# Optimization experiments

Hardware: AMD Instinct MI355X
Metric: run time of the kernel (lower is better)

## Reference

```python
import jax, jax.numpy as jnp
import numpy as np

D_MODEL = 512
N_LAYERS = 4
VOCAB = 256
SEQ = 2048
BATCH = 8
EPS = 1e-5


def _ln(x, g, b):
    mu = jnp.mean(x, axis=-1, keepdims=True)
    var = jnp.mean(jnp.square(x - mu), axis=-1, keepdims=True)
    return (x - mu) * jax.lax.rsqrt(var + EPS) * g + b


def setup_inputs() -> dict:
    key = jax.random.key(0)
    ks = jax.random.split(key, 16)
    d, dff = D_MODEL, 4 * D_MODEL
    s = 0.02
    inp = {
        "tokens": jax.random.randint(ks[0], (BATCH, SEQ), 0, VOCAB, dtype=jnp.int64),
        "emb": jax.random.normal(ks[1], (VOCAB, d), jnp.float32) * s,
        "W_upd": jax.random.normal(ks[2], (d, d), jnp.float32) * s,
        "b_upd": jnp.zeros((d,), jnp.float32),
        "W_f": jax.random.normal(ks[3], (d, d), jnp.float32) * s,
        "b_f": jnp.zeros((d,), jnp.float32),
        "decay_param": jnp.zeros((1,), jnp.float32),
        "norm_g": jnp.ones((d,), jnp.float32),
        "norm_b": jnp.zeros((d,), jnp.float32),
        "cms_ln_g": jnp.ones((N_LAYERS, d), jnp.float32),
        "cms_ln_b": jnp.zeros((N_LAYERS, d), jnp.float32),
        "cms_W1": jax.random.normal(ks[4], (N_LAYERS, d, dff), jnp.float32) * s,
        "cms_b1": jnp.zeros((N_LAYERS, dff), jnp.float32),
        "cms_W2": jax.random.normal(ks[5], (N_LAYERS, dff, d), jnp.float32) * s,
        "cms_b2": jnp.zeros((N_LAYERS, d), jnp.float32),
        "head_W": jax.random.normal(ks[6], (d, VOCAB), jnp.float32) * s,
        "head_b": jnp.zeros((VOCAB,), jnp.float32),
    }
    return inp


def _fast_memory(x, mask, W_upd, b_upd, W_f, b_f, decay_param):
    # x: (B,S,d), mask: (B,S) float
    decay = jax.nn.sigmoid(decay_param[0])
    u = jnp.einsum("bsd,de->bse", x, W_upd) + b_upd  # precompute updates
    u_t = jnp.swapaxes(u, 0, 1)                        # (S,B,d)
    m_t = jnp.swapaxes(mask, 0, 1)[..., None]          # (S,B,1)

    def step(mem, inp):
        u_i, msk = inp
        new = decay * mem + u_i
        mem = msk * new + (1.0 - msk) * mem
        return mem, mem

    mem0 = jnp.zeros((x.shape[0], x.shape[2]), x.dtype)
    _, mems = jax.lax.scan(step, mem0, (u_t, m_t))     # (S,B,d)
    mems = jnp.swapaxes(mems, 0, 1)                    # (B,S,d)
    return jnp.einsum("bsd,de->bse", mems, W_f) + b_f


def reference(tokens, emb, W_upd, b_upd, W_f, b_f, decay_param, norm_g, norm_b,
              cms_ln_g, cms_ln_b, cms_W1, cms_b1, cms_W2, cms_b2, head_W, head_b):
    mask = (tokens != 0).astype(emb.dtype)
    x = emb[tokens]                                    # (B,S,d)
    x = x + _fast_memory(x, mask, W_upd, b_upd, W_f, b_f, decay_param)
    x = _ln(x, norm_g, norm_b)
    for i in range(N_LAYERS):
        h = _ln(x, cms_ln_g[i], cms_ln_b[i])
        h = jax.nn.gelu(jnp.einsum("bsd,df->bsf", h, cms_W1[i]) + cms_b1[i], approximate=False)
        h = jnp.einsum("bsf,fd->bsd", h, cms_W2[i]) + cms_b2[i]
        x = x + h
    return jnp.einsum("bsd,dv->bsv", x, head_W) + head_b
```

## Files before the change

### kernel.cpp

```cpp
#include <hip/hip_runtime.h>
#include <hip/hip_bf16.h>
#include <math.h>

#define D_MODEL 512
#define N_LAYERS 4
#define SEQ 2048
#define BATCH 8
#define M_TOT (BATCH * SEQ)
#define DFF 2048
#define HEAD_V 256
#define SC 32
#define NC (SEQ / SC)

typedef __hip_bfloat16 bf16;
typedef __bf16 bf16x8 __attribute__((ext_vector_type(8)));
typedef float f32x4 __attribute__((ext_vector_type(4)));

__device__ __forceinline__ unsigned short bfbits(float x) {
    bf16 h = __float2bfloat16(x);
    return *(unsigned short*)&h;
}
__device__ __forceinline__ unsigned int pk(float a, float b) {
    return (unsigned int)bfbits(a) | ((unsigned int)bfbits(b) << 16);
}

__global__ void convT_kernel(const float* __restrict__ W, bf16* __restrict__ WT,
                             int R, int C, size_t wstride, size_t tstride) {
    W += (size_t)blockIdx.z * wstride;
    WT += (size_t)blockIdx.z * tstride;
    __shared__ float t[32][33];
    int r0 = blockIdx.x * 32, c0 = blockIdx.y * 32;
    int tx = threadIdx.x, ty = threadIdx.y;
    #pragma unroll
    for (int i = 0; i < 32; i += 8)
        t[ty + i][tx] = W[(size_t)(r0 + ty + i) * C + c0 + tx];
    __syncthreads();
    #pragma unroll
    for (int i = 0; i < 32; i += 8)
        WT[(size_t)(c0 + ty + i) * R + r0 + tx] = __float2bfloat16(t[tx][ty + i]);
}

__global__ void embed_kernel(const int* __restrict__ tokens,
                             const float* __restrict__ emb,
                             float* __restrict__ xf, bf16* __restrict__ xb) {
    int row = blockIdx.x, t = threadIdx.x;
    int tok = tokens[row];
    float4 v = ((const float4*)(emb + (size_t)tok * D_MODEL))[t];
    ((float4*)(xf + (size_t)row * D_MODEL))[t] = v;
    uint2 st; st.x = pk(v.x, v.y); st.y = pk(v.z, v.w);
    ((uint2*)(xb + (size_t)row * D_MODEL))[t] = st;
}

__global__ void scanA_kernel(bf16* __restrict__ u, const int* __restrict__ tokens,
                             const float* __restrict__ decayp,
                             float* __restrict__ L, float* __restrict__ P) {
    int idx = blockIdx.x;
    int dblk = idx & 1;
    int c = (idx >> 1) & (NC - 1);
    int b = idx >> 7;
    int d = dblk * 256 + threadIdx.x;
    float decay = 1.0f / (1.0f + __expf(-decayp[0]));
    const int* tok = tokens + (size_t)b * SEQ + c * SC;
    bf16* up = u + ((size_t)b * SEQ + (size_t)c * SC) * D_MODEL + d;
    float mem = 0.0f;
    #pragma unroll 4
    for (int s = 0; s < SC; ++s) {
        float ui = __bfloat162float(up[(size_t)s * D_MODEL]);
        bool m = (tok[s] != 0);
        mem = (m ? decay : 1.0f) * mem + (m ? ui : 0.0f);
        up[(size_t)s * D_MODEL] = __float2bfloat16(mem);
    }
    L[((size_t)b * NC + c) * D_MODEL + d] = mem;
    if (threadIdx.x == 0 && dblk == 0) {
        int cnt = 0;
        for (int s = 0; s < SC; ++s) cnt += (tok[s] != 0);
        P[b * NC + c] = __powf(decay, (float)cnt);
    }
}

__global__ void scanB_kernel(const float* __restrict__ L, const float* __restrict__ P,
                             float* __restrict__ Mc) {
    int b = blockIdx.x >> 1;
    int d = (blockIdx.x & 1) * 256 + threadIdx.x;
    float carry = 0.0f;
    for (int c = 0; c < NC; ++c) {
        size_t off = ((size_t)b * NC + c) * D_MODEL + d;
        Mc[off] = carry;
        carry = P[b * NC + c] * carry + L[off];
    }
}

__global__ void scanC_kernel(bf16* __restrict__ u, const int* __restrict__ tokens,
                             const float* __restrict__ decayp,
                             const float* __restrict__ Mc) {
    int idx = blockIdx.x;
    int dblk = idx & 1;
    int c = (idx >> 1) & (NC - 1);
    int b = idx >> 7;
    if (c == 0) return;
    int d = dblk * 256 + threadIdx.x;
    float decay = 1.0f / (1.0f + __expf(-decayp[0]));
    const int* tok = tokens + (size_t)b * SEQ + c * SC;
    bf16* up = u + ((size_t)b * SEQ + (size_t)c * SC) * D_MODEL + d;
    float carry = Mc[((size_t)b * NC + c) * D_MODEL + d];
    float coeff = 1.0f;
    #pragma unroll 4
    for (int s = 0; s < SC; ++s) {
        bool m = (tok[s] != 0);
        coeff *= (m ? decay : 1.0f);
        float local = __bfloat162float(up[(size_t)s * D_MODEL]);
        up[(size_t)s * D_MODEL] = __float2bfloat16(local + carry * coeff);
    }
}

template <int WF, int WB>
__global__ void ln_kernel(const float* __restrict__ in, float* __restrict__ outf,
                          bf16* __restrict__ outb, const float* __restrict__ g,
                          const float* __restrict__ b) {
    int w = threadIdx.x >> 6, lane = threadIdx.x & 63;
    int row = blockIdx.x * 4 + w;
    const float4* ip = (const float4*)(in + (size_t)row * D_MODEL);
    float4 v0 = ip[lane * 2], v1 = ip[lane * 2 + 1];
    float s1 = v0.x + v0.y + v0.z + v0.w + v1.x + v1.y + v1.z + v1.w;
    float s2 = v0.x * v0.x + v0.y * v0.y + v0.z * v0.z + v0.w * v0.w +
               v1.x * v1.x + v1.y * v1.y + v1.z * v1.z + v1.w * v1.w;
    #pragma unroll
    for (int off = 32; off; off >>= 1) {
        s1 += __shfl_xor(s1, off);
        s2 += __shfl_xor(s2, off);
    }
    float mu = s1 * (1.0f / D_MODEL);
    float var = s2 * (1.0f / D_MODEL) - mu * mu;
    float rstd = rsqrtf(var + 1e-5f);
    const float4* g4 = (const float4*)g;
    const float4* b4 = (const float4*)b;
    float4 g0 = g4[lane * 2], g1 = g4[lane * 2 + 1];
    float4 b0 = b4[lane * 2], b1 = b4[lane * 2 + 1];
    float4 o0, o1;
    o0.x = (v0.x - mu) * rstd * g0.x + b0.x;
    o0.y = (v0.y - mu) * rstd * g0.y + b0.y;
    o0.z = (v0.z - mu) * rstd * g0.z + b0.z;
    o0.w = (v0.w - mu) * rstd * g0.w + b0.w;
    o1.x = (v1.x - mu) * rstd * g1.x + b1.x;
    o1.y = (v1.y - mu) * rstd * g1.y + b1.y;
    o1.z = (v1.z - mu) * rstd * g1.z + b1.z;
    o1.w = (v1.w - mu) * rstd * g1.w + b1.w;
    if (WF) {
        float4* op = (float4*)(outf + (size_t)row * D_MODEL);
        op[lane * 2] = o0; op[lane * 2 + 1] = o1;
    }
    if (WB) {
        uint4 st;
        st.x = pk(o0.x, o0.y); st.y = pk(o0.z, o0.w);
        st.z = pk(o1.x, o1.y); st.w = pk(o1.z, o1.w);
        ((uint4*)(outb + (size_t)row * D_MODEL))[lane] = st;
    }
}

template <int BN, int GELU, int RES, int OBF>
__launch_bounds__(256)
__global__ void gemm_bf16(const bf16* __restrict__ A, const bf16* __restrict__ BT,
                          const float* __restrict__ bias, const float* __restrict__ R,
                          float* __restrict__ Cf, bf16* __restrict__ Cb,
                          int N, int K) {
    constexpr int NJ = BN / 32;
    __shared__ bf16 As[128 * 32];
    __shared__ bf16 Bs[BN * 32];
    const int tid = threadIdx.x;
    const int lane = tid & 63;
    const int w = tid >> 6, wr = w >> 1, wc = w & 1;
    const int lm = lane & 15, lk = lane >> 4;
    const int m0 = blockIdx.x * 128, n0 = blockIdx.y * BN;

    f32x4 acc[4][NJ] = {};

    for (int k0 = 0; k0 < K; k0 += 32) {
        #pragma unroll
        for (int it = 0; it < 2; ++it) {
            int c = tid + it * 256;
            __builtin_amdgcn_global_load_lds(
                A + (size_t)(m0 + (c >> 2)) * K + k0 + (c & 3) * 8,
                (char*)As + (c & ~63) * 16, 16, 0, 0);
        }
        #pragma unroll
        for (int it = 0; it < BN / 64; ++it) {
            int c = tid + it * 256;
            __builtin_amdgcn_global_load_lds(
                BT + (size_t)(n0 + (c >> 2)) * K + k0 + (c & 3) * 8,
                (char*)Bs + (c & ~63) * 16, 16, 0, 0);
        }
        __syncthreads();
        bf16x8 fa[4], fb[NJ];
        #pragma unroll
        for (int i = 0; i < 4; ++i)
            fa[i] = *(const bf16x8*)(As + (wr * 64 + i * 16 + lm) * 32 + lk * 8);
        #pragma unroll
        for (int j = 0; j < NJ; ++j)
            fb[j] = *(const bf16x8*)(Bs + (wc * (BN / 2) + j * 16 + lm) * 32 + lk * 8);
        #pragma unroll
        for (int i = 0; i < 4; ++i)
            #pragma unroll
            for (int j = 0; j < NJ; ++j)
                acc[i][j] = __builtin_amdgcn_mfma_f32_16x16x32_bf16(fa[i], fb[j], acc[i][j], 0, 0, 0);
        __syncthreads();
    }

    #pragma unroll
    for (int j = 0; j < NJ; ++j) {
        int col = n0 + wc * (BN / 2) + j * 16 + lm;
        float bv = bias[col];
        #pragma unroll
        for (int i = 0; i < 4; ++i) {
            int rbase = m0 + wr * 64 + i * 16 + lk * 4;
            #pragma unroll
            for (int r = 0; r < 4; ++r) {
                float v = acc[i][j][r] + bv;
                if (GELU) v = 0.5f * v * (1.0f + erff(v * 0.70710678118654752f));
                size_t off = (size_t)(rbase + r) * N + col;
                if (RES) v += R[off];
                if (OBF == 1) {
                    Cb[off] = __float2bfloat16(v);
                } else if (OBF == 2) {
                    Cf[off] = v;
                    Cb[off] = __float2bfloat16(v);
                } else {
                    Cf[off] = v;
                }
            }
        }
    }
}

extern "C" void kernel_launch(void* const* d_in, const int* in_sizes, int n_in,
                              void* d_out, int out_size, void* d_ws, size_t ws_size,
                              hipStream_t stream) {
    const int*   tokens = (const int*)d_in[0];
    const float* emb    = (const float*)d_in[1];
    const float* W_upd  = (const float*)d_in[2];
    const float* b_upd  = (const float*)d_in[3];
    const float* W_f    = (const float*)d_in[4];
    const float* b_f    = (const float*)d_in[5];
    const float* decayp = (const float*)d_in[6];
    const float* norm_g = (const float*)d_in[7];
    const float* norm_b = (const float*)d_in[8];
    const float* cms_g  = (const float*)d_in[9];
    const float* cms_b  = (const float*)d_in[10];
    const float* cW1    = (const float*)d_in[11];
    const float* cb1    = (const float*)d_in[12];
    const float* cW2    = (const float*)d_in[13];
    const float* cb2    = (const float*)d_in[14];
    const float* head_W = (const float*)d_in[15];
    const float* head_b = (const float*)d_in[16];
    float* out = (float*)d_out;

    const int M = M_TOT, D = D_MODEL, F = DFF, V = HEAD_V;

    float* xf = (float*)d_ws;
    bf16*  lnb = (bf16*)((char*)d_ws + (size_t)M * D * 4);
    bf16*  wb  = (bf16*)((char*)lnb + (size_t)M * D * 2);
    const size_t WB_ELEMS = 9043968;
    char* dyn = (char*)wb + WB_ELEMS * 2;
    size_t used = (size_t)(dyn - (char*)d_ws);
    size_t avail = ws_size > used ? ws_size - used : 0;
    int MC = 4096;
    if (avail >= (size_t)16384 * F * 2) MC = 16384;
    else if (avail >= (size_t)8192 * F * 2) MC = 8192;
    bf16* ub = (bf16*)dyn;
    bf16* hb = (bf16*)dyn;

    float* scanL = out;
    float* scanM = out + (size_t)BATCH * NC * D;
    float* scanP = scanM + (size_t)BATCH * NC * D;

    bf16* WupdT = wb;
    bf16* WfT   = wb + 262144;
    bf16* W1T   = wb + 524288;
    bf16* W2T   = wb + 4718592;
    bf16* HWT   = wb + 8912896;

    dim3 tb(32, 8);
    convT_kernel<<<dim3(16, 16, 2), tb, 0, stream>>>(W_upd, WupdT, D, D,
                                                     (size_t)(W_f - W_upd), 262144);
    convT_kernel<<<dim3(16, 64, N_LAYERS), tb, 0, stream>>>(cW1, W1T, D, F,
                                                            (size_t)D * F, 1048576);
    convT_kernel<<<dim3(64, 16, N_LAYERS), tb, 0, stream>>>(cW2, W2T, F, D,
                                                            (size_t)F * D, 1048576);
    convT_kernel<<<dim3(16, 8, 1), tb, 0, stream>>>(head_W, HWT, D, V, 0, 0);

    embed_kernel<<<M, 128, 0, stream>>>(tokens, emb, xf, lnb);

    gemm_bf16<128, 0, 0, 1><<<dim3(M / 128, D / 128), 256, 0, stream>>>(
        lnb, WupdT, b_upd, nullptr, nullptr, ub, D, D);
    scanA_kernel<<<BATCH * NC * 2, 256, 0, stream>>>(ub, tokens, decayp, scanL, scanP);
    scanB_kernel<<<BATCH * 2, 256, 0, stream>>>(scanL, scanP, scanM);
    scanC_kernel<<<BATCH * NC * 2, 256, 0, stream>>>(ub, tokens, decayp, scanM);
    gemm_bf16<128, 0, 1, 0><<<dim3(M / 128, D / 128), 256, 0, stream>>>(
        ub, WfT, b_f, xf, xf, nullptr, D, D);
    ln_kernel<1, 0><<<M / 4, 256, 0, stream>>>(xf, xf, nullptr, norm_g, norm_b);

    for (int l = 0; l < N_LAYERS; ++l) {
        ln_kernel<0, 1><<<M / 4, 256, 0, stream>>>(xf, nullptr, lnb,
                                                   cms_g + (size_t)l * D,
                                                   cms_b + (size_t)l * D);
        bool last = (l == N_LAYERS - 1);
        for (int mc = 0; mc < M; mc += MC) {
            gemm_bf16<128, 1, 0, 1><<<dim3(MC / 128, F / 128), 256, 0, stream>>>(
                lnb + (size_t)mc * D, W1T + (size_t)l * 1048576,
                cb1 + (size_t)l * F, nullptr, nullptr, hb, F, D);
            if (MC >= 8192) {
                if (last)
                    gemm_bf16<128, 0, 1, 2><<<dim3(MC / 128, D / 128), 256, 0, stream>>>(
                        hb, W2T + (size_t)l * 1048576, cb2 + (size_t)l * D,
                        xf + (size_t)mc * D, xf + (size_t)mc * D,
                        lnb + (size_t)mc * D, D, F);
                else
                    gemm_bf16<128, 0, 1, 0><<<dim3(MC / 128, D / 128), 256, 0, stream>>>(
                        hb, W2T + (size_t)l * 1048576, cb2 + (size_t)l * D,
                        xf + (size_t)mc * D, xf + (size_t)mc * D, nullptr, D, F);
            } else {
                if (last)
                    gemm_bf16<64, 0, 1, 2><<<dim3(MC / 128, D / 64), 256, 0, stream>>>(
                        hb, W2T + (size_t)l * 1048576, cb2 + (size_t)l * D,
                        xf + (size_t)mc * D, xf + (size_t)mc * D,
                        lnb + (size_t)mc * D, D, F);
                else
                    gemm_bf16<64, 0, 1, 0><<<dim3(MC / 128, D / 64), 256, 0, stream>>>(
                        hb, W2T + (size_t)l * 1048576, cb2 + (size_t)l * D,
                        xf + (size_t)mc * D, xf + (size_t)mc * D, nullptr, D, F);
            }
        }
    }

    gemm_bf16<128, 0, 0, 0><<<dim3(M / 128, V / 128), 256, 0, stream>>>(
        lnb, HWT, head_b, nullptr, out, nullptr, V, D);
}
```

Before: 660.5 us.

## Double-buffer GEMM LDS tiles and stage epilogue through LDS for vector stores

The GEMM main loop now keeps two LDS buffers and prefetches the next K tile with global_load_lds while MFMAs run on the current one. This replaces the two __syncthreads per iteration with a single wait plus barrier. The epilogue writes each warp's accumulators to LDS, then reads them back row-contiguous so bias, residual and outputs use float4 and uint4 accesses instead of scalar strided ones. The change doubles shared memory per block, which may reduce occupancy. Template kernels are also wrapped into named non-template kernels.

Result: faster. 584.9 us (-11.5%).

```diff
diff --git a/kernel.cpp b/kernel.cpp
--- a/kernel.cpp
+++ b/kernel.cpp
@@ -113,10 +113,12 @@
     }
 }
 
-template <int WF, int WB>
-__global__ void ln_kernel(const float* __restrict__ in, float* __restrict__ outf,
-                          bf16* __restrict__ outb, const float* __restrict__ g,
-                          const float* __restrict__ b) {
+__device__ __forceinline__ void ln_body(const float* __restrict__ in,
+                                        float* __restrict__ outf,
+                                        bf16* __restrict__ outb,
+                                        const float* __restrict__ g,
+                                        const float* __restrict__ b,
+                                        int WF, int WB) {
     int w = threadIdx.x >> 6, lane = threadIdx.x & 63;
     int row = blockIdx.x * 4 + w;
     const float4* ip = (const float4*)(in + (size_t)row * D_MODEL);
@@ -157,15 +159,44 @@
     }
 }
 
+__global__ void ln_f32_kernel(const float* __restrict__ in, float* __restrict__ outf,
+                              const float* __restrict__ g, const float* __restrict__ b) {
+    ln_body(in, outf, nullptr, g, b, 1, 0);
+}
+__global__ void ln_b16_kernel(const float* __restrict__ in, bf16* __restrict__ outb,
+                              const float* __restrict__ g, const float* __restrict__ b) {
+    ln_body(in, nullptr, outb, g, b, 0, 1);
+}
+
+#define STAGE(s, k0)                                                          \
+    do {                                                                      \
+        _Pragma("unroll")                                                     \
+        for (int it = 0; it < 2; ++it) {                                      \
+            int c = tid + it * 256;                                           \
+            __builtin_amdgcn_global_load_lds(                                 \
+                A + (size_t)(m0 + (c >> 2)) * K + (k0) + (c & 3) * 8,         \
+                smem + (s) * ABYTES + (c & ~63) * 16, 16, 0, 0);              \
+        }                                                                     \
+        _Pragma("unroll")                                                     \
+        for (int it = 0; it < LB; ++it) {                                     \
+            int c = tid + it * 256;                                           \
+            __builtin_amdgcn_global_load_lds(                                 \
+                BT + (size_t)(n0 + (c >> 2)) * K + (k0) + (c & 3) * 8,        \
+                smem + 2 * ABYTES + (s) * BBYTES + (c & ~63) * 16, 16, 0, 0); \
+        }                                                                     \
+    } while (0)
+
 template <int BN, int GELU, int RES, int OBF>
-__launch_bounds__(256)
-__global__ void gemm_bf16(const bf16* __restrict__ A, const bf16* __restrict__ BT,
+__device__ __forceinline__ void gemm_body(char* smem,
+                          const bf16* __restrict__ A, const bf16* __restrict__ BT,
                           const float* __restrict__ bias, const float* __restrict__ R,
                           float* __restrict__ Cf, bf16* __restrict__ Cb,
                           int N, int K) {
     constexpr int NJ = BN / 32;
-    __shared__ bf16 As[128 * 32];
-    __shared__ bf16 Bs[BN * 32];
+    constexpr int LB = BN / 64;
+    constexpr int ABYTES = 128 * 32 * 2;
+    constexpr int BBYTES = BN * 32 * 2;
+    constexpr int ST = 16 * NJ + 4;
     const int tid = threadIdx.x;
     const int lane = tid & 63;
     const int w = tid >> 6, wr = w >> 1, wc = w & 1;
@@ -174,62 +205,101 @@
 
     f32x4 acc[4][NJ] = {};
 
-    for (int k0 = 0; k0 < K; k0 += 32) {
-        #pragma unroll
-        for (int it = 0; it < 2; ++it) {
-            int c = tid + it * 256;
-            __builtin_amdgcn_global_load_lds(
-                A + (size_t)(m0 + (c >> 2)) * K + k0 + (c & 3) * 8,
-                (char*)As + (c & ~63) * 16, 16, 0, 0);
-        }
-        #pragma unroll
-        for (int it = 0; it < BN / 64; ++it) {
-            int c = tid + it * 256;
-            __builtin_amdgcn_global_load_lds(
-                BT + (size_t)(n0 + (c >> 2)) * K + k0 + (c & 3) * 8,
-                (char*)Bs + (c & ~63) * 16, 16, 0, 0);
-        }
-        __syncthreads();
+    const int nt = K / 32;
+    STAGE(0, 0);
+    asm volatile("s_waitcnt vmcnt(0)" ::: "memory");
+    __builtin_amdgcn_s_barrier();
+    __builtin_amdgcn_sched_barrier(0);
+    int cur = 0;
+    for (int t = 0; t < nt; ++t) {
+        if (t + 1 < nt) STAGE(cur ^ 1, (t + 1) * 32);
+        const bf16* Asc = (const bf16*)(smem + cur * ABYTES);
+        const bf16* Bsc = (const bf16*)(smem + 2 * ABYTES + cur * BBYTES);
         bf16x8 fa[4], fb[NJ];
         #pragma unroll
         for (int i = 0; i < 4; ++i)
-            fa[i] = *(const bf16x8*)(As + (wr * 64 + i * 16 + lm) * 32 + lk * 8);
+            fa[i] = *(const bf16x8*)(Asc + (wr * 64 + i * 16 + lm) * 32 + lk * 8);
         #pragma unroll
         for (int j = 0; j < NJ; ++j)
-            fb[j] = *(const bf16x8*)(Bs + (wc * (BN / 2) + j * 16 + lm) * 32 + lk * 8);
+            fb[j] = *(const bf16x8*)(Bsc + (wc * (BN / 2) + j * 16 + lm) * 32 + lk * 8);
         #pragma unroll
         for (int i = 0; i < 4; ++i)
             #pragma unroll
             for (int j = 0; j < NJ; ++j)
                 acc[i][j] = __builtin_amdgcn_mfma_f32_16x16x32_bf16(fa[i], fb[j], acc[i][j], 0, 0, 0);
-        __syncthreads();
-    }
-
+        asm volatile("s_waitcnt vmcnt(0)" ::: "memory");
+        __builtin_amdgcn_s_barrier();
+        __builtin_amdgcn_sched_barrier(0);
+        cur ^= 1;
+    }
+
+    float* ep = (float*)smem + w * 16 * ST;
+    const int r2 = lane >> 2;
+    const int q = lane & 3;
+    constexpr int CW = 16 * NJ;
+    const int gc0 = n0 + wc * CW + q * 4 * NJ;
     #pragma unroll
-    for (int j = 0; j < NJ; ++j) {
-        int col = n0 + wc * (BN / 2) + j * 16 + lm;
-        float bv = bias[col];
-        #pragma unroll
-        for (int i = 0; i < 4; ++i) {
-            int rbase = m0 + wr * 64 + i * 16 + lk * 4;
+    for (int i = 0; i < 4; ++i) {
+        #pragma unroll
+        for (int j = 0; j < NJ; ++j)
             #pragma unroll
-            for (int r = 0; r < 4; ++r) {
-                float v = acc[i][j][r] + bv;
-                if (GELU) v = 0.5f * v * (1.0f + erff(v * 0.70710678118654752f));
-                size_t off = (size_t)(rbase + r) * N + col;
-                if (RES) v += R[off];
-                if (OBF == 1) {
-                    Cb[off] = __float2bfloat16(v);
-                } else if (OBF == 2) {
-                    Cf[off] = v;
-                    Cb[off] = __float2bfloat16(v);
-                } else {
-                    Cf[off] = v;
-                }
+            for (int r = 0; r < 4; ++r)
+                ep[(lk * 4 + r) * ST + j * 16 + lm] = acc[i][j][r];
+        int grow = m0 + wr * 64 + i * 16 + r2;
+        float4 fx[NJ];
+        #pragma unroll
+        for (int v = 0; v < NJ; ++v)
+            fx[v] = *(const float4*)&ep[r2 * ST + q * 4 * NJ + v * 4];
+        #pragma unroll
+        for (int v = 0; v < NJ; ++v) {
+            float4 bb = *(const float4*)(bias + gc0 + v * 4);
+            fx[v].x += bb.x; fx[v].y += bb.y; fx[v].z += bb.z; fx[v].w += bb.w;
+            if (GELU) {
+                fx[v].x = 0.5f * fx[v].x * (1.0f + erff(fx[v].x * 0.70710678118654752f));
+                fx[v].y = 0.5f * fx[v].y * (1.0f + erff(fx[v].y * 0.70710678118654752f));
+                fx[v].z = 0.5f * fx[v].z * (1.0f + erff(fx[v].z * 0.70710678118654752f));
+                fx[v].w = 0.5f * fx[v].w * (1.0f + erff(fx[v].w * 0.70710678118654752f));
+            }
+            if (RES) {
+                float4 rr = *(const float4*)(R + (size_t)grow * N + gc0 + v * 4);
+                fx[v].x += rr.x; fx[v].y += rr.y; fx[v].z += rr.z; fx[v].w += rr.w;
             }
         }
-    }
-}
+        if (OBF == 0 || OBF == 2) {
+            #pragma unroll
+            for (int v = 0; v < NJ; ++v)
+                *(float4*)(Cf + (size_t)grow * N + gc0 + v * 4) = fx[v];
+        }
+        if (OBF >= 1) {
+            #pragma unroll
+            for (int v = 0; v < NJ; v += 2) {
+                uint4 st;
+                st.x = pk(fx[v].x, fx[v].y);
+                st.y = pk(fx[v].z, fx[v].w);
+                st.z = pk(fx[v + 1].x, fx[v + 1].y);
+                st.w = pk(fx[v + 1].z, fx[v + 1].w);
+                *(uint4*)(Cb + (size_t)grow * N + gc0 + v * 4) = st;
+            }
+        }
+    }
+}
+
+#define DEF_GEMM(name, BN, GELU, RES, OBF)                                    \
+__launch_bounds__(256) __global__ void name(                                  \
+        const bf16* __restrict__ A, const bf16* __restrict__ BT,              \
+        const float* __restrict__ bias, const float* __restrict__ R,          \
+        float* __restrict__ Cf, bf16* __restrict__ Cb, int N, int K) {        \
+    __shared__ char smem[16384 + (BN) * 128];                                 \
+    gemm_body<BN, GELU, RES, OBF>(smem, A, BT, bias, R, Cf, Cb, N, K);        \
+}
+
+DEF_GEMM(gemm_u,       128, 0, 0, 1)
+DEF_GEMM(gemm_res,     128, 0, 1, 0)
+DEF_GEMM(gemm_gelu,    128, 1, 0, 1)
+DEF_GEMM(gemm_resboth, 128, 0, 1, 2)
+DEF_GEMM(gemm_plain,   128, 0, 0, 0)
+DEF_GEMM(gemm64_res,      64, 0, 1, 0)
+DEF_GEMM(gemm64_resboth,  64, 0, 1, 2)
 
 extern "C" void kernel_launch(void* const* d_in, const int* in_sizes, int n_in,
                               void* d_out, int out_size, void* d_ws, size_t ws_size,
@@ -289,48 +359,48 @@
 
     embed_kernel<<<M, 128, 0, stream>>>(tokens, emb, xf, lnb);
 
-    gemm_bf16<128, 0, 0, 1><<<dim3(M / 128, D / 128), 256, 0, stream>>>(
+    gemm_u<<<dim3(M / 128, D / 128), 256, 0, stream>>>(
         lnb, WupdT, b_upd, nullptr, nullptr, ub, D, D);
     scanA_kernel<<<BATCH * NC * 2, 256, 0, stream>>>(ub, tokens, decayp, scanL, scanP);
     scanB_kernel<<<BATCH * 2, 256, 0, stream>>>(scanL, scanP, scanM);
     scanC_kernel<<<BATCH * NC * 2, 256, 0, stream>>>(ub, tokens, decayp, scanM);
-    gemm_bf16<128, 0, 1, 0><<<dim3(M / 128, D / 128), 256, 0, stream>>>(
+    gemm_res<<<dim3(M / 128, D / 128), 256, 0, stream>>>(
         ub, WfT, b_f, xf, xf, nullptr, D, D);
-    ln_kernel<1, 0><<<M / 4, 256, 0, stream>>>(xf, xf, nullptr, norm_g, norm_b);
+    ln_f32_kernel<<<M / 4, 256, 0, stream>>>(xf, xf, norm_g, norm_b);
 
     for (int l = 0; l < N_LAYERS; ++l) {
-        ln_kernel<0, 1><<<M / 4, 256, 0, stream>>>(xf, nullptr, lnb,
-                                                   cms_g + (size_t)l * D,
-                                                   cms_b + (size_t)l * D);
+        ln_b16_kernel<<<M / 4, 256, 0, stream>>>(xf, lnb,
+                                                 cms_g + (size_t)l * D,
+                                                 cms_b + (size_t)l * D);
         bool last = (l == N_LAYERS - 1);
         for (int mc = 0; mc < M; mc += MC) {
-            gemm_bf16<128, 1, 0, 1><<<dim3(MC / 128, F / 128), 256, 0, stream>>>(
+            gemm_gelu<<<dim3(MC / 128, F / 128), 256, 0, stream>>>(
                 lnb + (size_t)mc * D, W1T + (size_t)l * 1048576,
                 cb1 + (size_t)l * F, nullptr, nullptr, hb, F, D);
             if (MC >= 8192) {
                 if (last)
-                    gemm_bf16<128, 0, 1, 2><<<dim3(MC / 128, D / 128), 256, 0, stream>>>(
+                    gemm_resboth<<<dim3(MC / 128, D / 128), 256, 0, stream>>>(
                         hb, W2T + (size_t)l * 1048576, cb2 + (size_t)l * D,
                         xf + (size_t)mc * D, xf + (size_t)mc * D,
                         lnb + (size_t)mc * D, D, F);
                 else
-                    gemm_bf16<128, 0, 1, 0><<<dim3(MC / 128, D / 128), 256, 0, stream>>>(
+                    gemm_res<<<dim3(MC / 128, D / 128), 256, 0, stream>>>(
                         hb, W2T + (size_t)l * 1048576, cb2 + (size_t)l * D,
                         xf + (size_t)mc * D, xf + (size_t)mc * D, nullptr, D, F);
             } else {
                 if (last)
-                    gemm_bf16<64, 0, 1, 2><<<dim3(MC / 128, D / 64), 256, 0, stream>>>(
+                    gemm64_resboth<<<dim3(MC / 128, D / 64), 256, 0, stream>>>(
                         hb, W2T + (size_t)l * 1048576, cb2 + (size_t)l * D,
                         xf + (size_t)mc * D, xf + (size_t)mc * D,
                         lnb + (size_t)mc * D, D, F);
                 else
-                    gemm_bf16<64, 0, 1, 0><<<dim3(MC / 128, D / 64), 256, 0, stream>>>(
+                    gemm64_res<<<dim3(MC / 128, D / 64), 256, 0, stream>>>(
                         hb, W2T + (size_t)l * 1048576, cb2 + (size_t)l * D,
                         xf + (size_t)mc * D, xf + (size_t)mc * D, nullptr, D, F);
             }
         }
     }
 
-    gemm_bf16<128, 0, 0, 0><<<dim3(M / 128, V / 128), 256, 0, stream>>>(
+    gemm_plain<<<dim3(M / 128, V / 128), 256, 0, stream>>>(
         lnb, HWT, head_b, nullptr, out, nullptr, V, D);
 }
```
